# Optimization experiments

Measured on AMD Instinct MI355X. Metric: run time of the kernel, lower is better.

## Reference

```python
import jax, jax.numpy as jnp
import numpy as np

N0, N1, N2 = 2_000_000, 200_000, 16_384
D_IN, D_HID, D_OUT = 128, 32, 64
E0, E1 = 3_200_000, 262_144


def setup_inputs() -> dict:
    key = jax.random.key(0)
    ks = jax.random.split(key, 9)
    x = jax.random.normal(ks[0], (N0, D_IN), dtype=jnp.float32)
    edge_src0 = jax.random.randint(ks[1], (E0,), 0, N0)
    edge_dst0 = jax.random.randint(ks[2], (E0,), 0, N1)
    edge_src1 = jax.random.randint(ks[3], (E1,), 0, N1)
    edge_dst1 = jax.random.randint(ks[4], (E1,), 0, N2)
    s = lambda d: (1.0 / np.sqrt(d)).astype(np.float32)
    W1l = jax.random.normal(ks[5], (D_HID, D_IN), dtype=jnp.float32) * s(D_IN)
    W1r = jax.random.normal(ks[6], (D_HID, D_IN), dtype=jnp.float32) * s(D_IN)
    W2l = jax.random.normal(ks[7], (D_OUT, D_HID), dtype=jnp.float32) * s(D_HID)
    W2r = jax.random.normal(ks[8], (D_OUT, D_HID), dtype=jnp.float32) * s(D_HID)
    return {"x": x, "W1l": W1l, "W1r": W1r, "W2l": W2l, "W2r": W2r,
            "edge_src0": edge_src0, "edge_dst0": edge_dst0,
            "edge_src1": edge_src1, "edge_dst1": edge_dst1}


def _sage_conv(x_src, x_dst, src, dst, Wl, Wr, n_dst):
    # mean aggregation of source features onto destination nodes
    msg = x_src[src]                                            # [E, d]
    agg = jax.ops.segment_sum(msg, dst, num_segments=n_dst)     # [n_dst, d]
    cnt = jax.ops.segment_sum(jnp.ones_like(dst, dtype=x_src.dtype), dst,
                              num_segments=n_dst)
    mean = agg / jnp.maximum(cnt, 1.0)[:, None]
    # out = lin_l(mean) + lin_r(x_dst), no bias
    return mean @ Wl.T + x_dst @ Wr.T


def reference(x, W1l, W1r, W2l, W2r, edge_src0, edge_dst0, edge_src1, edge_dst1):
    # layer 0: N0 -> N1
    h = _sage_conv(x, x[:N1], edge_src0, edge_dst0, W1l, W1r, N1)
    h = jax.nn.relu(h)  # dropout is identity at inference
    # layer 1: N1 -> N2
    out = _sage_conv(h, h[:N2], edge_src1, edge_dst1, W2l, W2r, N2)
    return out
```

## Files before the change

kernel.cpp:

```cpp
#include <hip/hip_runtime.h>
#include <hip/hip_bf16.h>

#define N0 2000000
#define N1 200000
#define N2 16384
#define D_IN 128
#define D_HID 32
#define D_OUT 64
#define E0 3200000
#define E1 262144

typedef __attribute__((ext_vector_type(8))) short bf16x8;
typedef __attribute__((ext_vector_type(4))) float floatx4;

__device__ __forceinline__ short f2bf(float f) {
  unsigned u = __float_as_uint(f);
  u += 0x7FFFu + ((u >> 16) & 1u);
  return (short)(u >> 16);
}

__global__ __launch_bounds__(256, 2) void k_project0(
    const float* __restrict__ x, const float* __restrict__ W1l,
    const float* __restrict__ W1r, float* __restrict__ z0,
    float* __restrict__ r0) {
  const int lane = threadIdx.x & 63;
  const int quad = lane >> 4;
  const int r15 = lane & 15;
  const int wid = (int)((blockIdx.x * blockDim.x + threadIdx.x) >> 6);
  const int nwaves = (int)((gridDim.x * blockDim.x) >> 6);

  bf16x8 Bf[4][4];
#pragma unroll
  for (int nt = 0; nt < 4; ++nt) {
    int n = nt * 16 + r15;
    const float* wrow = (n < 32) ? (W1l + n * 128) : (W1r + (n - 32) * 128);
#pragma unroll
    for (int ks = 0; ks < 4; ++ks) {
      const float* p = wrow + ks * 32 + quad * 8;
#pragma unroll
      for (int j = 0; j < 8; ++j) Bf[nt][ks][j] = f2bf(p[j]);
    }
  }

  const int ntiles = N0 / 16;
  for (int t = wid; t < ntiles; t += nwaves) {
    const int row0 = t * 16;
    const float* xrow = x + (size_t)(row0 + r15) * 128 + quad * 8;
    bf16x8 Af[4];
#pragma unroll
    for (int ks = 0; ks < 4; ++ks) {
      const float* p = xrow + ks * 32;
#pragma unroll
      for (int j = 0; j < 8; ++j) Af[ks][j] = f2bf(p[j]);
    }
    const bool full = (row0 < N1);
    floatx4 acc[4] = {{0.f,0.f,0.f,0.f},{0.f,0.f,0.f,0.f},
                      {0.f,0.f,0.f,0.f},{0.f,0.f,0.f,0.f}};
#pragma unroll
    for (int nt = 0; nt < 4; ++nt) {
      if (nt < 2 || full) {
#pragma unroll
        for (int ks = 0; ks < 4; ++ks)
          acc[nt] = __builtin_amdgcn_mfma_f32_16x16x32_bf16(
              Af[ks], Bf[nt][ks], acc[nt], 0, 0, 0);
      }
    }
#pragma unroll
    for (int nt = 0; nt < 2; ++nt) {
      int col = nt * 16 + r15;
#pragma unroll
      for (int i = 0; i < 4; ++i) {
        int row = row0 + quad * 4 + i;
        z0[(size_t)row * 32 + col] = acc[nt][i];
      }
    }
    if (full) {
#pragma unroll
      for (int nt = 2; nt < 4; ++nt) {
        int col = (nt - 2) * 16 + r15;
#pragma unroll
        for (int i = 0; i < 4; ++i) {
          int row = row0 + quad * 4 + i;
          r0[(size_t)row * 32 + col] = acc[nt][i];
        }
      }
    }
  }
}

__global__ void k_edge0(const int* __restrict__ src, const int* __restrict__ dst,
                        const float* __restrict__ z0, float* __restrict__ agg0,
                        float* __restrict__ cnt0) {
  long tid = (long)blockIdx.x * blockDim.x + threadIdx.x;
  long e = tid >> 5;
  int j = (int)(tid & 31);
  if (e < E0) {
    int s = src[e], d = dst[e];
    float v = z0[(size_t)s * 32 + j];
    unsafeAtomicAdd(&agg0[(size_t)d * 32 + j], v);
    if (j == 0) unsafeAtomicAdd(&cnt0[d], 1.0f);
  }
}

__global__ __launch_bounds__(256) void k_hidden(
    const float* __restrict__ agg0, const float* __restrict__ cnt0,
    const float* __restrict__ r0, const float* __restrict__ W2l,
    const float* __restrict__ W2r, float* __restrict__ z1,
    float* __restrict__ r1) {
  const int lane = threadIdx.x & 63;
  const int wid = (int)((blockIdx.x * blockDim.x + threadIdx.x) >> 6);
  const int nwaves = (int)((gridDim.x * blockDim.x) >> 6);
  float wl[32], wr[32];
#pragma unroll
  for (int j = 0; j < 32; ++j) {
    wl[j] = W2l[lane * 32 + j];
    wr[j] = W2r[lane * 32 + j];
  }
  const int l32 = lane & 31;
  for (int i = wid; i < N1; i += nwaves) {
    float a = agg0[(size_t)i * 32 + l32];
    float r = r0[(size_t)i * 32 + l32];
    float c = cnt0[i];
    float h = fmaxf(a / fmaxf(c, 1.0f) + r, 0.0f);
    float az = 0.f, ar = 0.f;
#pragma unroll
    for (int j = 0; j < 32; ++j) {
      float hj = __shfl(h, j, 64);
      az = fmaf(hj, wl[j], az);
      ar = fmaf(hj, wr[j], ar);
    }
    z1[(size_t)i * 64 + lane] = az;
    if (i < N2) r1[(size_t)i * 64 + lane] = ar;
  }
}

__global__ void k_edge1(const int* __restrict__ src, const int* __restrict__ dst,
                        const float* __restrict__ z1, float* __restrict__ agg1,
                        float* __restrict__ cnt1) {
  long tid = (long)blockIdx.x * blockDim.x + threadIdx.x;
  long e = tid >> 6;
  int j = (int)(tid & 63);
  if (e < E1) {
    int s = src[e], d = dst[e];
    float v = z1[(size_t)s * 64 + j];
    unsafeAtomicAdd(&agg1[(size_t)d * 64 + j], v);
    if (j == 0) unsafeAtomicAdd(&cnt1[d], 1.0f);
  }
}

__global__ void k_out(const float* __restrict__ agg1,
                      const float* __restrict__ cnt1,
                      const float* __restrict__ r1, float* __restrict__ out) {
  int tid = (int)(blockIdx.x * blockDim.x + threadIdx.x);
  if (tid < N2 * 64) {
    int i = tid >> 6;
    out[tid] = agg1[tid] / fmaxf(cnt1[i], 1.0f) + r1[tid];
  }
}

extern "C" void kernel_launch(void* const* d_in, const int* in_sizes, int n_in,
                              void* d_out, int out_size, void* d_ws,
                              size_t ws_size, hipStream_t stream) {
  const float* x   = (const float*)d_in[0];
  const float* W1l = (const float*)d_in[1];
  const float* W1r = (const float*)d_in[2];
  const float* W2l = (const float*)d_in[3];
  const float* W2r = (const float*)d_in[4];
  const int* es0 = (const int*)d_in[5];
  const int* ed0 = (const int*)d_in[6];
  const int* es1 = (const int*)d_in[7];
  const int* ed1 = (const int*)d_in[8];
  float* out = (float*)d_out;

  float* ws = (float*)d_ws;
  float* z0 = ws;
  float* r0 = z0 + (size_t)N0 * 32;
  float* z1 = r0 + (size_t)N1 * 32;
  float* r1 = z1 + (size_t)N1 * 64;
  float* agg0 = r1 + (size_t)N2 * 64;
  float* cnt0 = agg0 + (size_t)N1 * 32;
  float* agg1 = cnt0 + N1;
  float* cnt1 = agg1 + (size_t)N2 * 64;

  size_t zero_bytes =
      ((size_t)N1 * 32 + N1 + (size_t)N2 * 64 + N2) * sizeof(float);
  hipMemsetAsync(agg0, 0, zero_bytes, stream);

  k_project0<<<1024, 256, 0, stream>>>(x, W1l, W1r, z0, r0);
  k_edge0<<<(E0 * 32) / 256, 256, 0, stream>>>(es0, ed0, z0, agg0, cnt0);
  k_hidden<<<1024, 256, 0, stream>>>(agg0, cnt0, r0, W2l, W2r, z1, r1);
  k_edge1<<<(E1 * 64) / 256, 256, 0, stream>>>(es1, ed1, z1, agg1, cnt1);
  k_out<<<(N2 * 64) / 256, 256, 0, stream>>>(agg1, cnt1, r1, out);
}
```

Before: 1.987 ms.

## Replace atomic scatter with CSR gather aggregation and bf16 intermediates

Builds a CSR by destination (histogram, scan, fill) for both layers, so aggregation becomes a per-destination gather-sum without float atomics. The projected features z0, h and z1 are stored as bf16 to halve gather traffic, and the second projection uses MFMA instead of shuffle FMAs. In exchange it adds several small launches and a CSR build that still uses integer atomics, and bf16 storage of the intermediates loses some precision.

```diff
diff --git a/kernel.cpp b/kernel.cpp
--- a/kernel.cpp
+++ b/kernel.cpp
@@ -18,10 +18,13 @@
   u += 0x7FFFu + ((u >> 16) & 1u);
   return (short)(u >> 16);
 }
+__device__ __forceinline__ float bf2f(unsigned short u) {
+  return __uint_as_float(((unsigned)u) << 16);
+}
 
 __global__ __launch_bounds__(256, 2) void k_project0(
     const float* __restrict__ x, const float* __restrict__ W1l,
-    const float* __restrict__ W1r, float* __restrict__ z0,
+    const float* __restrict__ W1r, unsigned short* __restrict__ z0h,
     float* __restrict__ r0) {
   const int lane = threadIdx.x & 63;
   const int quad = lane >> 4;
@@ -71,7 +74,7 @@
 #pragma unroll
       for (int i = 0; i < 4; ++i) {
         int row = row0 + quad * 4 + i;
-        z0[(size_t)row * 32 + col] = acc[nt][i];
+        z0h[(size_t)row * 32 + col] = (unsigned short)f2bf(acc[nt][i]);
       }
     }
     if (full) {
@@ -88,74 +91,181 @@
   }
 }
 
-__global__ void k_edge0(const int* __restrict__ src, const int* __restrict__ dst,
-                        const float* __restrict__ z0, float* __restrict__ agg0,
-                        float* __restrict__ cnt0) {
-  long tid = (long)blockIdx.x * blockDim.x + threadIdx.x;
-  long e = tid >> 5;
-  int j = (int)(tid & 31);
-  if (e < E0) {
-    int s = src[e], d = dst[e];
-    float v = z0[(size_t)s * 32 + j];
-    unsafeAtomicAdd(&agg0[(size_t)d * 32 + j], v);
-    if (j == 0) unsafeAtomicAdd(&cnt0[d], 1.0f);
-  }
-}
-
-__global__ __launch_bounds__(256) void k_hidden(
-    const float* __restrict__ agg0, const float* __restrict__ cnt0,
-    const float* __restrict__ r0, const float* __restrict__ W2l,
-    const float* __restrict__ W2r, float* __restrict__ z1,
+__global__ void k_hist(const int* __restrict__ dst, int n, int* __restrict__ deg) {
+  int e = (int)(blockIdx.x * blockDim.x + threadIdx.x);
+  if (e < n) atomicAdd(&deg[dst[e]], 1);
+}
+
+__global__ __launch_bounds__(256) void k_scan1(const int* __restrict__ deg, int n,
+                                               int* __restrict__ rs,
+                                               int* __restrict__ bsum) {
+  __shared__ int buf[2][256];
+  const int t = threadIdx.x;
+  const int base = (int)blockIdx.x * 1024 + t * 4;
+  int v[4];
+  int s = 0;
+#pragma unroll
+  for (int j = 0; j < 4; ++j) {
+    v[j] = (base + j < n) ? deg[base + j] : 0;
+    s += v[j];
+  }
+  buf[0][t] = s;
+  __syncthreads();
+  int cur = 0;
+  for (int off = 1; off < 256; off <<= 1) {
+    int val = buf[cur][t] + ((t >= off) ? buf[cur][t - off] : 0);
+    buf[1 - cur][t] = val;
+    __syncthreads();
+    cur = 1 - cur;
+  }
+  int incl = buf[cur][t];
+  int run = incl - s;
+  if (t == 255) bsum[blockIdx.x] = incl;
+#pragma unroll
+  for (int j = 0; j < 4; ++j) {
+    if (base + j < n) rs[base + j] = run;
+    run += v[j];
+  }
+}
+
+__global__ __launch_bounds__(256) void k_scan2(int* __restrict__ bsum, int n) {
+  __shared__ int buf[2][256];
+  const int t = threadIdx.x;
+  int s = (t < n) ? bsum[t] : 0;
+  buf[0][t] = s;
+  __syncthreads();
+  int cur = 0;
+  for (int off = 1; off < 256; off <<= 1) {
+    int val = buf[cur][t] + ((t >= off) ? buf[cur][t - off] : 0);
+    buf[1 - cur][t] = val;
+    __syncthreads();
+    cur = 1 - cur;
+  }
+  if (t < n) bsum[t] = buf[cur][t] - s;
+}
+
+__global__ void k_scan3(int* __restrict__ rs, const int* __restrict__ bsum, int n) {
+  int i = (int)(blockIdx.x * blockDim.x + threadIdx.x);
+  if (i < n) rs[i] += bsum[i >> 10];
+}
+
+__global__ void k_fill(const int* __restrict__ src, const int* __restrict__ dst,
+                       int n, int* __restrict__ rs, int* __restrict__ csr) {
+  int e = (int)(blockIdx.x * blockDim.x + threadIdx.x);
+  if (e < n) {
+    int p = atomicAdd(&rs[dst[e]], 1);
+    csr[p] = src[e];
+  }
+}
+
+__global__ __launch_bounds__(256) void k_agg0(
+    const unsigned short* __restrict__ z0h, const int* __restrict__ csr,
+    const int* __restrict__ rs, const int* __restrict__ deg,
+    const float* __restrict__ r0, unsigned short* __restrict__ hb) {
+  const int lane = threadIdx.x & 63;
+  const int col = lane & 31;
+  const int half = lane >> 5;
+  const int i = (int)((blockIdx.x * blockDim.x + threadIdx.x) >> 6);
+  const int d = deg[i];
+  const int base = rs[i] - d;
+  float a0 = 0.f, a1 = 0.f;
+  int k = half;
+  for (; k + 2 < d; k += 4) {
+    int s0 = csr[base + k];
+    int s1 = csr[base + k + 2];
+    a0 += bf2f(z0h[(size_t)s0 * 32 + col]);
+    a1 += bf2f(z0h[(size_t)s1 * 32 + col]);
+  }
+  for (; k < d; k += 2) {
+    int s = csr[base + k];
+    a0 += bf2f(z0h[(size_t)s * 32 + col]);
+  }
+  float acc = a0 + a1;
+  acc += __shfl_xor(acc, 32, 64);
+  float h = fmaxf(acc / fmaxf((float)d, 1.0f) + r0[(size_t)i * 32 + col], 0.0f);
+  if (half == 0) hb[(size_t)i * 32 + col] = (unsigned short)f2bf(h);
+}
+
+__global__ __launch_bounds__(256, 2) void k_proj1(
+    const unsigned short* __restrict__ hb, const float* __restrict__ W2l,
+    const float* __restrict__ W2r, unsigned short* __restrict__ z1b,
     float* __restrict__ r1) {
   const int lane = threadIdx.x & 63;
+  const int quad = lane >> 4;
+  const int r15 = lane & 15;
   const int wid = (int)((blockIdx.x * blockDim.x + threadIdx.x) >> 6);
   const int nwaves = (int)((gridDim.x * blockDim.x) >> 6);
-  float wl[32], wr[32];
-#pragma unroll
-  for (int j = 0; j < 32; ++j) {
-    wl[j] = W2l[lane * 32 + j];
-    wr[j] = W2r[lane * 32 + j];
-  }
-  const int l32 = lane & 31;
-  for (int i = wid; i < N1; i += nwaves) {
-    float a = agg0[(size_t)i * 32 + l32];
-    float r = r0[(size_t)i * 32 + l32];
-    float c = cnt0[i];
-    float h = fmaxf(a / fmaxf(c, 1.0f) + r, 0.0f);
-    float az = 0.f, ar = 0.f;
-#pragma unroll
-    for (int j = 0; j < 32; ++j) {
-      float hj = __shfl(h, j, 64);
-      az = fmaf(hj, wl[j], az);
-      ar = fmaf(hj, wr[j], ar);
-    }
-    z1[(size_t)i * 64 + lane] = az;
-    if (i < N2) r1[(size_t)i * 64 + lane] = ar;
-  }
-}
-
-__global__ void k_edge1(const int* __restrict__ src, const int* __restrict__ dst,
-                        const float* __restrict__ z1, float* __restrict__ agg1,
-                        float* __restrict__ cnt1) {
-  long tid = (long)blockIdx.x * blockDim.x + threadIdx.x;
-  long e = tid >> 6;
-  int j = (int)(tid & 63);
-  if (e < E1) {
-    int s = src[e], d = dst[e];
-    float v = z1[(size_t)s * 64 + j];
-    unsafeAtomicAdd(&agg1[(size_t)d * 64 + j], v);
-    if (j == 0) unsafeAtomicAdd(&cnt1[d], 1.0f);
-  }
-}
-
-__global__ void k_out(const float* __restrict__ agg1,
-                      const float* __restrict__ cnt1,
-                      const float* __restrict__ r1, float* __restrict__ out) {
-  int tid = (int)(blockIdx.x * blockDim.x + threadIdx.x);
-  if (tid < N2 * 64) {
-    int i = tid >> 6;
-    out[tid] = agg1[tid] / fmaxf(cnt1[i], 1.0f) + r1[tid];
-  }
+
+  bf16x8 Bf[8];
+#pragma unroll
+  for (int nt = 0; nt < 8; ++nt) {
+    int n = (nt & 3) * 16 + r15;
+    const float* wrow = (nt < 4) ? (W2l + n * 32) : (W2r + n * 32);
+#pragma unroll
+    for (int j = 0; j < 8; ++j) Bf[nt][j] = f2bf(wrow[quad * 8 + j]);
+  }
+
+  const int ntiles = N1 / 16;
+  for (int t = wid; t < ntiles; t += nwaves) {
+    const int row0 = t * 16;
+    bf16x8 Af = *(const bf16x8*)(hb + (size_t)(row0 + r15) * 32 + quad * 8);
+    const bool doR = (row0 < N2);
+    floatx4 acc[8];
+#pragma unroll
+    for (int nt = 0; nt < 8; ++nt) acc[nt] = (floatx4){0.f, 0.f, 0.f, 0.f};
+#pragma unroll
+    for (int nt = 0; nt < 4; ++nt)
+      acc[nt] = __builtin_amdgcn_mfma_f32_16x16x32_bf16(Af, Bf[nt], acc[nt], 0, 0, 0);
+    if (doR) {
+#pragma unroll
+      for (int nt = 4; nt < 8; ++nt)
+        acc[nt] = __builtin_amdgcn_mfma_f32_16x16x32_bf16(Af, Bf[nt], acc[nt], 0, 0, 0);
+    }
+#pragma unroll
+    for (int nt = 0; nt < 4; ++nt) {
+      int col = nt * 16 + r15;
+#pragma unroll
+      for (int i = 0; i < 4; ++i) {
+        int row = row0 + quad * 4 + i;
+        z1b[(size_t)row * 64 + col] = (unsigned short)f2bf(acc[nt][i]);
+      }
+    }
+    if (doR) {
+#pragma unroll
+      for (int nt = 4; nt < 8; ++nt) {
+        int col = (nt - 4) * 16 + r15;
+#pragma unroll
+        for (int i = 0; i < 4; ++i) {
+          int row = row0 + quad * 4 + i;
+          r1[(size_t)row * 64 + col] = acc[nt][i];
+        }
+      }
+    }
+  }
+}
+
+__global__ __launch_bounds__(256) void k_agg1(
+    const unsigned short* __restrict__ z1b, const int* __restrict__ csr,
+    const int* __restrict__ rs, const int* __restrict__ deg,
+    const float* __restrict__ r1, float* __restrict__ out) {
+  const int lane = threadIdx.x & 63;
+  const int i = (int)((blockIdx.x * blockDim.x + threadIdx.x) >> 6);
+  const int d = deg[i];
+  const int base = rs[i] - d;
+  float a0 = 0.f, a1 = 0.f;
+  int k = 0;
+  for (; k + 1 < d; k += 2) {
+    int s0 = csr[base + k];
+    int s1 = csr[base + k + 1];
+    a0 += bf2f(z1b[(size_t)s0 * 64 + lane]);
+    a1 += bf2f(z1b[(size_t)s1 * 64 + lane]);
+  }
+  if (k < d) {
+    int s = csr[base + k];
+    a0 += bf2f(z1b[(size_t)s * 64 + lane]);
+  }
+  out[(size_t)i * 64 + lane] =
+      (a0 + a1) / fmaxf((float)d, 1.0f) + r1[(size_t)i * 64 + lane];
 }
 
 extern "C" void kernel_launch(void* const* d_in, const int* in_sizes, int n_in,
@@ -172,23 +282,45 @@
   const int* ed1 = (const int*)d_in[8];
   float* out = (float*)d_out;
 
-  float* ws = (float*)d_ws;
-  float* z0 = ws;
-  float* r0 = z0 + (size_t)N0 * 32;
-  float* z1 = r0 + (size_t)N1 * 32;
-  float* r1 = z1 + (size_t)N1 * 64;
-  float* agg0 = r1 + (size_t)N2 * 64;
-  float* cnt0 = agg0 + (size_t)N1 * 32;
-  float* agg1 = cnt0 + N1;
-  float* cnt1 = agg1 + (size_t)N2 * 64;
-
-  size_t zero_bytes =
-      ((size_t)N1 * 32 + N1 + (size_t)N2 * 64 + N2) * sizeof(float);
-  hipMemsetAsync(agg0, 0, zero_bytes, stream);
-
-  k_project0<<<1024, 256, 0, stream>>>(x, W1l, W1r, z0, r0);
-  k_edge0<<<(E0 * 32) / 256, 256, 0, stream>>>(es0, ed0, z0, agg0, cnt0);
-  k_hidden<<<1024, 256, 0, stream>>>(agg0, cnt0, r0, W2l, W2r, z1, r1);
-  k_edge1<<<(E1 * 64) / 256, 256, 0, stream>>>(es1, ed1, z1, agg1, cnt1);
-  k_out<<<(N2 * 64) / 256, 256, 0, stream>>>(agg1, cnt1, r1, out);
-}
+  char* p = (char*)d_ws;
+  auto alloc = [&](size_t bytes) {
+    char* q = p;
+    p += (bytes + 255) & ~(size_t)255;
+    return q;
+  };
+  unsigned short* z0h = (unsigned short*)alloc((size_t)N0 * 32 * 2);
+  unsigned short* hb  = (unsigned short*)alloc((size_t)N1 * 32 * 2);
+  unsigned short* z1b = (unsigned short*)alloc((size_t)N1 * 64 * 2);
+  float* r0 = (float*)alloc((size_t)N1 * 32 * 4);
+  float* r1 = (float*)alloc((size_t)N2 * 64 * 4);
+  int* csr0 = (int*)alloc((size_t)E0 * 4);
+  int* csr1 = (int*)alloc((size_t)E1 * 4);
+  int* rs0  = (int*)alloc((size_t)N1 * 4);
+  int* rs1  = (int*)alloc((size_t)N2 * 4);
+  int* deg0 = (int*)alloc((size_t)(N1 + N2) * 4);
+  int* deg1 = deg0 + N1;
+  int* bsum0 = (int*)alloc(256 * 4);
+  int* bsum1 = (int*)alloc(256 * 4);
+
+  hipMemsetAsync(deg0, 0, (size_t)(N1 + N2) * 4, stream);
+
+  const int nb0 = (N1 + 1023) / 1024;
+  const int nb1 = (N2 + 1023) / 1024;
+
+  k_project0<<<1024, 256, 0, stream>>>(x, W1l, W1r, z0h, r0);
+
+  k_hist<<<(E0 + 255) / 256, 256, 0, stream>>>(ed0, E0, deg0);
+  k_hist<<<(E1 + 255) / 256, 256, 0, stream>>>(ed1, E1, deg1);
+  k_scan1<<<nb0, 256, 0, stream>>>(deg0, N1, rs0, bsum0);
+  k_scan1<<<nb1, 256, 0, stream>>>(deg1, N2, rs1, bsum1);
+  k_scan2<<<1, 256, 0, stream>>>(bsum0, nb0);
+  k_scan2<<<1, 256, 0, stream>>>(bsum1, nb1);
+  k_scan3<<<(N1 + 255) / 256, 256, 0, stream>>>(rs0, bsum0, N1);
+  k_scan3<<<(N2 + 255) / 256, 256, 0, stream>>>(rs1, bsum1, N2);
+  k_fill<<<(E0 + 255) / 256, 256, 0, stream>>>(es0, ed0, E0, rs0, csr0);
+  k_fill<<<(E1 + 255) / 256, 256, 0, stream>>>(es1, ed1, E1, rs1, csr1);
+
+  k_agg0<<<N1 / 4, 256, 0, stream>>>(z0h, csr0, rs0, deg0, r0, hb);
+  k_proj1<<<1024, 256, 0, stream>>>(hb, W2l, W2r, z1b, r1);
+  k_agg1<<<N2 / 4, 256, 0, stream>>>(z1b, csr1, rs1, deg1, r1, out);
+}
```

Result: no change. 1.960 ms (-1.4%).
